# Performance work log

Measured on AMD Instinct MI355X. Metric: run time of the kernel, lower is better.

## Reference

```python
import jax, jax.numpy as jnp
import numpy as np

CLAMP_LO, CLAMP_HI = 0.001, 0.999
GUMBEL_SEED = 42


def setup_inputs() -> dict:
    key = jax.random.key(0)
    k0, k1, k2, k3 = jax.random.split(key, 4)
    B, N, F = 16, 1024, 128
    nodes = jax.random.normal(k0, (B, N, F), dtype=jnp.float32)
    adj = jnp.zeros((B, N, N), dtype=jnp.float32)
    weights = jnp.zeros((B, N, N), dtype=jnp.float32)
    num_nodes = jax.random.randint(k1, (B,), 0, 1023)
    # edge network params: Linear(2F, F) -> LeakyReLU -> Linear(F, 1) -> Sigmoid
    W1 = jax.random.normal(k2, (2 * F, F), dtype=jnp.float32) / np.sqrt(2 * F).astype(np.float32)
    b1 = jnp.zeros((F,), dtype=jnp.float32)
    W2 = jax.random.normal(k3, (F, 1), dtype=jnp.float32) / np.sqrt(F).astype(np.float32)
    b2 = jnp.zeros((1,), dtype=jnp.float32)
    return {"nodes": nodes, "adj": adj, "weights": weights, "num_nodes": num_nodes,
            "B": B, "W1": W1, "b1": b1, "W2": W2, "b2": b2}


def _edge_mlp(x, W1, b1, W2, b2):
    h = jax.nn.leaky_relu(x @ W1 + b1)  # default torch negative_slope = 0.01
    return jax.nn.sigmoid(h @ W2 + b2)


def reference(nodes, adj, weights, num_nodes, B, W1, b1, W2, b2):
    # adj input is overwritten by the module; unused.
    Bn, N, F = nodes.shape
    # compute_logits2: left = nodes[b, num_nodes[b]], right = nodes[b, i] for i < num_nodes[b]
    left = nodes[jnp.arange(Bn), num_nodes]                      # [B, F]
    net_in = jnp.concatenate(
        [jnp.broadcast_to(left[:, None, :], (Bn, N, F)), nodes], axis=-1)  # [B, N, 2F]
    probs = jnp.clip(_edge_mlp(net_in, W1, b1, W2, b2)[..., 0], CLAMP_LO, CLAMP_HI)  # [B, N]
    i_mask = jnp.arange(N)[None, :] < num_nodes[:, None]          # [B, N] valid i rows
    j_onehot = jnp.arange(N)[None, None, :] == num_nodes[:, None, None]  # [B, 1, N] column j
    sel = i_mask[:, :, None] & j_onehot                           # [B, N, N]
    w = jnp.where(sel, probs[:, :, None], weights)
    # sample_hard: gumbel-softmax (tau=1, hard) over stacked (1-p, p), keep class 1
    logits = jnp.log(jnp.clip(jnp.stack([1.0 - w, w], axis=0), CLAMP_LO, CLAMP_HI))  # [2,B,N,N]
    u = jax.random.uniform(jax.random.key(GUMBEL_SEED), logits.shape,
                           minval=1e-10, maxval=1.0)
    g = -jnp.log(-jnp.log(u))
    y_soft = jax.nn.softmax(logits + g, axis=0)
    hard1 = (jnp.argmax(y_soft, axis=0) == 1).astype(w.dtype)     # [B,N,N]
    adj_out = hard1 + y_soft[1] - jax.lax.stop_gradient(y_soft[1])  # straight-through
    return adj_out, w
```

## Files before the change

kernel.cpp:

```cpp
#include <hip/hip_runtime.h>
#include <stdint.h>

namespace {

constexpr int kB = 16;
constexpr int kN = 1024;
constexpr int kF = 128;
constexpr int kHalf = kB * kN * kN;
constexpr int kElems = 8;
constexpr int kScreenBlocks = kHalf / (256 * kElems);

typedef float f32x4 __attribute__((ext_vector_type(4)));

__device__ __forceinline__ uint32_t rotl32(uint32_t x, int r) {
  return __builtin_amdgcn_alignbit(x, x, 32 - r);
}

__device__ __forceinline__ void tf2x32(uint32_t x0, uint32_t x1,
                                       uint32_t& o0, uint32_t& o1) {
  constexpr uint32_t ks0 = 0u;
  constexpr uint32_t ks1 = 42u;
  constexpr uint32_t ks2 = 0u ^ 42u ^ 0x1BD11BDAu;
  x0 += ks0; x1 += ks1;
#define TFR(r) { x0 += x1; x1 = rotl32(x1, (r)); x1 ^= x0; }
  TFR(13) TFR(15) TFR(26) TFR(6)
  x0 += ks1; x1 += ks2 + 1u;
  TFR(17) TFR(29) TFR(16) TFR(24)
  x0 += ks2; x1 += ks0 + 2u;
  TFR(13) TFR(15) TFR(26) TFR(6)
  x0 += ks0; x1 += ks1 + 3u;
  TFR(17) TFR(29) TFR(16) TFR(24)
  x0 += ks1; x1 += ks2 + 4u;
  TFR(13) TFR(15) TFR(26) TFR(6)
  x0 += ks2; x1 += ks0 + 5u;
#undef TFR
  o0 = x0; o1 = x1;
}

__device__ __forceinline__ uint32_t random_bits_part(uint32_t idx) {
  uint32_t o0, o1;
  tf2x32(0u, idx, o0, o1);
  return o0 ^ o1;
}

__device__ __forceinline__ float bits_to_uniform(uint32_t bits) {
  float f = __uint_as_float((bits >> 9) | 0x3F800000u) - 1.0f;
  return fmaxf(1e-10f, f + 1e-10f);
}

__device__ __forceinline__ float decide_elem(uint32_t q, float c0, float c1) {
  const float u0 = bits_to_uniform(random_bits_part(q));
  const float u1 = bits_to_uniform(random_bits_part(q + (uint32_t)kHalf));
  const float lf0 = __log2f(u0);
  const float lf1 = __log2f(u1);
  const float D = c0 * lf1 - c1 * lf0;
  float r = (D > 0.0f) ? 1.0f : 0.0f;
  if (fabsf(D) <= 0.01f) {
    const float L0 = -logf(u0);
    const float L1 = -logf(u1);
    r = (c1 * L0 > c0 * L1) ? 1.0f : 0.0f;
  }
  return r;
}

__global__ __launch_bounds__(256) void mlp_probs_kernel(
    const float* __restrict__ nodes, const int* __restrict__ num_nodes,
    const float* __restrict__ W1, const float* __restrict__ b1,
    const float* __restrict__ W2, const float* __restrict__ b2,
    float* __restrict__ out_w) {
  __shared__ float xs[32][256];
  __shared__ float bt[16][128];
  __shared__ float hs[32][128];
  __shared__ float h2[32][8];

  const int blk = blockIdx.x;
  const int b = blk >> 5;
  const int i0 = (blk & 31) * 32;
  const int t = threadIdx.x;
  const int nn = num_nodes[b];
  if (i0 >= nn) return;
  const float* nb = nodes + (size_t)b * kN * kF;
  const float* leftp = nb + (size_t)nn * kF;

  for (int chunk = 0; chunk < 16; ++chunk) {
    int idx = chunk * 256 + t;
    int r = idx >> 7;
    int c = idx & 127;
    xs[r][c] = leftp[c];
    xs[r][128 + c] = nb[(size_t)(i0 + r) * kF + c];
  }

  const int tx = t & 31;
  const int ty = t >> 5;
  float acc[4][4];
#pragma unroll
  for (int rr = 0; rr < 4; ++rr)
#pragma unroll
    for (int cc = 0; cc < 4; ++cc) acc[rr][cc] = 0.0f;

  for (int k0 = 0; k0 < 256; k0 += 16) {
    __syncthreads();
#pragma unroll
    for (int qq = 0; qq < 8; ++qq) {
      int idx = qq * 256 + t;
      int kk = idx >> 7;
      int c = idx & 127;
      bt[kk][c] = W1[(size_t)(k0 + kk) * kF + c];
    }
    __syncthreads();
#pragma unroll
    for (int kk = 0; kk < 16; ++kk) {
      float bv0 = bt[kk][4 * tx + 0];
      float bv1 = bt[kk][4 * tx + 1];
      float bv2 = bt[kk][4 * tx + 2];
      float bv3 = bt[kk][4 * tx + 3];
#pragma unroll
      for (int rr = 0; rr < 4; ++rr) {
        float xv = xs[4 * ty + rr][k0 + kk];
        acc[rr][0] = fmaf(xv, bv0, acc[rr][0]);
        acc[rr][1] = fmaf(xv, bv1, acc[rr][1]);
        acc[rr][2] = fmaf(xv, bv2, acc[rr][2]);
        acc[rr][3] = fmaf(xv, bv3, acc[rr][3]);
      }
    }
  }

#pragma unroll
  for (int rr = 0; rr < 4; ++rr)
#pragma unroll
    for (int cc = 0; cc < 4; ++cc) {
      float v = acc[rr][cc] + b1[4 * tx + cc];
      hs[4 * ty + rr][4 * tx + cc] = (v >= 0.0f) ? v : 0.01f * v;
    }
  __syncthreads();

  {
    const int r = t >> 3;
    const int q = t & 7;
    float s = 0.0f;
#pragma unroll
    for (int j = 0; j < 16; ++j) {
      int k = q * 16 + j;
      s = fmaf(hs[r][k], W2[k], s);
    }
    h2[r][q] = s;
  }
  __syncthreads();

  if (t < 32) {
    float z = 0.0f;
#pragma unroll
    for (int q = 0; q < 8; ++q) z += h2[t][q];
    z += b2[0];
    double p = 1.0 / (1.0 + exp(-(double)z));
    float pc = fminf(fmaxf((float)p, 0.001f), 0.999f);
    out_w[(size_t)((b << 10) + i0 + t) * kN + nn] = pc;
  }
}

__global__ __launch_bounds__(256) void edge_screen_kernel(
    const float* __restrict__ weights, const int* __restrict__ num_nodes,
    float* __restrict__ out_adj, float* __restrict__ out_w) {
  __shared__ uint32_t s_cnt;
  __shared__ uint32_t s_q[256 * kElems];
  __shared__ float s_w[256 * kElems];
  if (threadIdx.x == 0) s_cnt = 0;
  __syncthreads();

  const int tid = blockIdx.x * 256 + threadIdx.x;
  const int q0 = tid * kElems;
  const int b = q0 >> 20;
  const int i = (q0 >> 10) & 1023;
  const int j0 = q0 & 1023;
  const int nn = num_nodes[b];
  const bool rowsel = (i < nn);
  const int rowbase = q0 - j0;

  float pv = 0.0f;
  if (rowsel && nn >= j0 && nn < j0 + kElems) pv = out_w[rowbase + nn];

  const float4 wqa = *reinterpret_cast<const float4*>(weights + q0);
  const float4 wqb = *reinterpret_cast<const float4*>(weights + q0 + 4);
  float wvals[kElems] = {wqa.x, wqa.y, wqa.z, wqa.w, wqb.x, wqb.y, wqb.z, wqb.w};
  float ow[kElems];

  constexpr uint32_t kBitsThr = (8190000u << 9) | 511u;

#pragma unroll
  for (int ee = 0; ee < kElems; ++ee) {
    const int j = j0 + ee;
    const float w = (rowsel && (j == nn)) ? pv : wvals[ee];
    const uint32_t bits =
        random_bits_part((uint32_t)(q0 + ee) + (uint32_t)kHalf);
    ow[ee] = w;
    if ((w != 0.0f) || (bits > kBitsThr)) {
      uint32_t k = atomicAdd(&s_cnt, 1u);
      s_q[k] = (uint32_t)(q0 + ee);
      s_w[k] = w;
    }
  }

  const float4 z4 = make_float4(0.0f, 0.0f, 0.0f, 0.0f);
  *reinterpret_cast<float4*>(out_adj + q0) = z4;
  *reinterpret_cast<float4*>(out_adj + q0 + 4) = z4;
  {
    f32x4 v0 = {ow[0], ow[1], ow[2], ow[3]};
    f32x4 v1 = {ow[4], ow[5], ow[6], ow[7]};
    __builtin_nontemporal_store(v0, reinterpret_cast<f32x4*>(out_w + q0));
    __builtin_nontemporal_store(v1, reinterpret_cast<f32x4*>(out_w + q0 + 4));
  }

  __syncthreads();

  const uint32_t n = s_cnt;
  for (uint32_t k = threadIdx.x; k < n; k += 256) {
    const uint32_t q = s_q[k];
    const float w = s_w[k];
    const float c1 = fminf(fmaxf(w, 0.001f), 0.999f);
    const float c0 = fminf(fmaxf(1.0f - w, 0.001f), 0.999f);
    if (decide_elem(q, c0, c1) > 0.5f) out_adj[q] = 1.0f;
  }
}

}

extern "C" void kernel_launch(void* const* d_in, const int* in_sizes, int n_in,
                              void* d_out, int out_size, void* d_ws, size_t ws_size,
                              hipStream_t stream) {
  (void)in_sizes; (void)n_in; (void)out_size; (void)d_ws; (void)ws_size;
  const float* nodes = (const float*)d_in[0];
  const float* weights = (const float*)d_in[2];
  const int* num_nodes = (const int*)d_in[3];
  const float* W1 = (const float*)d_in[5];
  const float* b1 = (const float*)d_in[6];
  const float* W2 = (const float*)d_in[7];
  const float* b2 = (const float*)d_in[8];

  float* out_adj = (float*)d_out;
  float* out_w = out_adj + (size_t)kHalf;

  hipLaunchKernelGGL(mlp_probs_kernel, dim3(512), dim3(256), 0, stream,
                     nodes, num_nodes, W1, b1, W2, b2, out_w);
  hipLaunchKernelGGL(edge_screen_kernel, dim3(kScreenBlocks), dim3(256), 0, stream,
                     weights, num_nodes, out_adj, out_w);
}
```

Measured before the change: 59.99 us.

## Run bulk screen first, then MLP, then patch the selected column

Reorders the pipeline so the bulk edge screen runs first, without needing num_nodes or the MLP probabilities. The MLP then overwrites the selected column of w, and a small per-batch patch kernel recomputes adj for those column entries. The screen also switches from per-lane shared-memory atomics to wave-level ballot/popcount compaction and drops the s_w buffer, reloading weights for survivors instead. This removes the dependency-driven per-element selection logic and cuts LDS atomic contention, at the cost of one extra launch and a serialized patch kernel with only 16 blocks.

```diff
diff --git a/kernel.cpp b/kernel.cpp
--- a/kernel.cpp
+++ b/kernel.cpp
@@ -63,6 +63,64 @@
   return r;
 }
 
+__global__ __launch_bounds__(256) void edge_screen_kernel(
+    const float* __restrict__ weights,
+    float* __restrict__ out_adj, float* __restrict__ out_w) {
+  __shared__ uint32_t s_cnt;
+  __shared__ uint32_t s_q[256 * kElems];
+  if (threadIdx.x == 0) s_cnt = 0;
+  __syncthreads();
+
+  const int tid = blockIdx.x * 256 + threadIdx.x;
+  const int q0 = tid * kElems;
+
+  const float4 wqa = *reinterpret_cast<const float4*>(weights + q0);
+  const float4 wqb = *reinterpret_cast<const float4*>(weights + q0 + 4);
+  float wvals[kElems] = {wqa.x, wqa.y, wqa.z, wqa.w, wqb.x, wqb.y, wqb.z, wqb.w};
+
+  constexpr uint32_t kBitsThr = (8190000u << 9) | 511u;
+
+#pragma unroll
+  for (int ee = 0; ee < kElems; ++ee) {
+    const uint32_t bits =
+        random_bits_part((uint32_t)(q0 + ee) + (uint32_t)kHalf);
+    const bool surv = (wvals[ee] != 0.0f) || (bits > kBitsThr);
+    const uint64_t m = __ballot(surv);
+    if (m != 0ull) {
+      uint32_t base = 0;
+      if ((threadIdx.x & 63) == 0)
+        base = atomicAdd(&s_cnt, (uint32_t)__popcll(m));
+      base = __builtin_amdgcn_readfirstlane(base);
+      if (surv) {
+        const uint32_t off = __builtin_amdgcn_mbcnt_hi(
+            (uint32_t)(m >> 32), __builtin_amdgcn_mbcnt_lo((uint32_t)m, 0u));
+        s_q[base + off] = (uint32_t)(q0 + ee);
+      }
+    }
+  }
+
+  const float4 z4 = make_float4(0.0f, 0.0f, 0.0f, 0.0f);
+  *reinterpret_cast<float4*>(out_adj + q0) = z4;
+  *reinterpret_cast<float4*>(out_adj + q0 + 4) = z4;
+  {
+    f32x4 v0 = {wvals[0], wvals[1], wvals[2], wvals[3]};
+    f32x4 v1 = {wvals[4], wvals[5], wvals[6], wvals[7]};
+    __builtin_nontemporal_store(v0, reinterpret_cast<f32x4*>(out_w + q0));
+    __builtin_nontemporal_store(v1, reinterpret_cast<f32x4*>(out_w + q0 + 4));
+  }
+
+  __syncthreads();
+
+  const uint32_t n = s_cnt;
+  for (uint32_t k = threadIdx.x; k < n; k += 256) {
+    const uint32_t q = s_q[k];
+    const float w = weights[q];
+    const float c1 = fminf(fmaxf(w, 0.001f), 0.999f);
+    const float c0 = fminf(fmaxf(1.0f - w, 0.001f), 0.999f);
+    if (decide_elem(q, c0, c1) > 0.5f) out_adj[q] = 1.0f;
+  }
+}
+
 __global__ __launch_bounds__(256) void mlp_probs_kernel(
     const float* __restrict__ nodes, const int* __restrict__ num_nodes,
     const float* __restrict__ W1, const float* __restrict__ b1,
@@ -147,7 +205,7 @@
   }
   __syncthreads();
 
-  if (t < 32) {
+  if (t < 32 && (i0 + t) < nn) {
     float z = 0.0f;
 #pragma unroll
     for (int q = 0; q < 8; ++q) z += h2[t][q];
@@ -158,67 +216,17 @@
   }
 }
 
-__global__ __launch_bounds__(256) void edge_screen_kernel(
-    const float* __restrict__ weights, const int* __restrict__ num_nodes,
-    float* __restrict__ out_adj, float* __restrict__ out_w) {
-  __shared__ uint32_t s_cnt;
-  __shared__ uint32_t s_q[256 * kElems];
-  __shared__ float s_w[256 * kElems];
-  if (threadIdx.x == 0) s_cnt = 0;
-  __syncthreads();
-
-  const int tid = blockIdx.x * 256 + threadIdx.x;
-  const int q0 = tid * kElems;
-  const int b = q0 >> 20;
-  const int i = (q0 >> 10) & 1023;
-  const int j0 = q0 & 1023;
+__global__ __launch_bounds__(256) void edge_patch_kernel(
+    const int* __restrict__ num_nodes,
+    float* __restrict__ out_adj, const float* __restrict__ out_w) {
+  const int b = blockIdx.x;
   const int nn = num_nodes[b];
-  const bool rowsel = (i < nn);
-  const int rowbase = q0 - j0;
-
-  float pv = 0.0f;
-  if (rowsel && nn >= j0 && nn < j0 + kElems) pv = out_w[rowbase + nn];
-
-  const float4 wqa = *reinterpret_cast<const float4*>(weights + q0);
-  const float4 wqb = *reinterpret_cast<const float4*>(weights + q0 + 4);
-  float wvals[kElems] = {wqa.x, wqa.y, wqa.z, wqa.w, wqb.x, wqb.y, wqb.z, wqb.w};
-  float ow[kElems];
-
-  constexpr uint32_t kBitsThr = (8190000u << 9) | 511u;
-
-#pragma unroll
-  for (int ee = 0; ee < kElems; ++ee) {
-    const int j = j0 + ee;
-    const float w = (rowsel && (j == nn)) ? pv : wvals[ee];
-    const uint32_t bits =
-        random_bits_part((uint32_t)(q0 + ee) + (uint32_t)kHalf);
-    ow[ee] = w;
-    if ((w != 0.0f) || (bits > kBitsThr)) {
-      uint32_t k = atomicAdd(&s_cnt, 1u);
-      s_q[k] = (uint32_t)(q0 + ee);
-      s_w[k] = w;
-    }
-  }
-
-  const float4 z4 = make_float4(0.0f, 0.0f, 0.0f, 0.0f);
-  *reinterpret_cast<float4*>(out_adj + q0) = z4;
-  *reinterpret_cast<float4*>(out_adj + q0 + 4) = z4;
-  {
-    f32x4 v0 = {ow[0], ow[1], ow[2], ow[3]};
-    f32x4 v1 = {ow[4], ow[5], ow[6], ow[7]};
-    __builtin_nontemporal_store(v0, reinterpret_cast<f32x4*>(out_w + q0));
-    __builtin_nontemporal_store(v1, reinterpret_cast<f32x4*>(out_w + q0 + 4));
-  }
-
-  __syncthreads();
-
-  const uint32_t n = s_cnt;
-  for (uint32_t k = threadIdx.x; k < n; k += 256) {
-    const uint32_t q = s_q[k];
-    const float w = s_w[k];
-    const float c1 = fminf(fmaxf(w, 0.001f), 0.999f);
-    const float c0 = fminf(fmaxf(1.0f - w, 0.001f), 0.999f);
-    if (decide_elem(q, c0, c1) > 0.5f) out_adj[q] = 1.0f;
+  for (int i = threadIdx.x; i < nn; i += 256) {
+    const uint32_t q = (uint32_t)((b << 20) + (i << 10) + nn);
+    const float p = out_w[q];
+    const float c1 = fminf(fmaxf(p, 0.001f), 0.999f);
+    const float c0 = fminf(fmaxf(1.0f - p, 0.001f), 0.999f);
+    out_adj[q] = decide_elem(q, c0, c1);
   }
 }
 
@@ -239,8 +247,10 @@
   float* out_adj = (float*)d_out;
   float* out_w = out_adj + (size_t)kHalf;
 
+  hipLaunchKernelGGL(edge_screen_kernel, dim3(kScreenBlocks), dim3(256), 0, stream,
+                     weights, out_adj, out_w);
   hipLaunchKernelGGL(mlp_probs_kernel, dim3(512), dim3(256), 0, stream,
                      nodes, num_nodes, W1, b1, W2, b2, out_w);
-  hipLaunchKernelGGL(edge_screen_kernel, dim3(kScreenBlocks), dim3(256), 0, stream,
-                     weights, num_nodes, out_adj, out_w);
-}
+  hipLaunchKernelGGL(edge_patch_kernel, dim3(kB), dim3(256), 0, stream,
+                     num_nodes, out_adj, out_w);
+}
```

Result: slower. 66.70 us (+11.2%).
